# Optimization experiments

Hardware: AMD Instinct MI355X
Metric: run time of the kernel (lower is better)

The kernel has to match this reference:

```python
import jax, jax.numpy as jnp
import numpy as np

B, L, D_MODEL = 2, 1024, 512
N_LAYERS, D_STATE, D_CONV = 6, 16, 4
D_INNER = 2 * D_MODEL          # Mamba default expand=2
DT_RANK = (D_MODEL + 15) // 16  # ceil(d_model/16) = 32
EPS = 1.1920929e-07             # torch RMSNorm default eps (fp32 machine eps)


def rmsnorm(x, w):
    return x * jax.lax.rsqrt(jnp.mean(x * x, axis=-1, keepdims=True) + EPS) * w


def selective_scan(u, dt, A, Bm, Cm, Dv):
    # u, dt: (B,L,E); A: (E,N); Bm, Cm: (B,L,N); Dv: (E,)
    dA = jnp.exp(jnp.einsum('ble,en->blen', dt, A))    # discretized A (ZOH)
    dBu = jnp.einsum('ble,bln->blen', dt * u, Bm)      # discretized B * u (Euler)

    def step(h, inp):
        dA_t, dBu_t, C_t = inp
        h = dA_t * h + dBu_t                           # (B,E,N) state update
        y = jnp.einsum('ben,bn->be', h, C_t)
        return h, y

    h0 = jnp.zeros((u.shape[0], u.shape[2], A.shape[1]), u.dtype)
    _, ys = jax.lax.scan(step, h0,
                         (dA.transpose(1, 0, 2, 3), dBu.transpose(1, 0, 2, 3),
                          Cm.transpose(1, 0, 2)))
    return ys.transpose(1, 0, 2) + u * Dv


def mamba_block(x, p):
    xz = jnp.einsum('bld,ed->ble', x, p['in_proj_w'])  # (B,L,2E)
    xi, z = jnp.split(xz, 2, axis=-1)
    # causal depthwise conv1d (kernel D_CONV) + bias + SiLU
    xc = jnp.pad(xi.transpose(0, 2, 1), ((0, 0), (0, 0), (D_CONV - 1, 0)))
    xc = jax.lax.conv_general_dilated(xc, p['conv_w'][:, None, :], (1,), 'VALID',
                                      feature_group_count=D_INNER)
    xi = jax.nn.silu(xc.transpose(0, 2, 1) + p['conv_b'])
    dbc = jnp.einsum('ble,re->blr', xi, p['x_proj_w'])  # (B,L,R+2N)
    dt, Bm, Cm = jnp.split(dbc, [DT_RANK, DT_RANK + D_STATE], axis=-1)
    dt = jax.nn.softplus(jnp.einsum('blr,er->ble', dt, p['dt_w']) + p['dt_b'])
    y = selective_scan(xi, dt, -jnp.exp(p['A_log']), Bm, Cm, p['D'])
    y = y * jax.nn.silu(z)                              # gate branch
    return jnp.einsum('ble,de->bld', y, p['out_w'])


def setup_inputs() -> dict:
    key = jax.random.key(0)
    ks = jax.random.split(key, 8)
    s = 0.02
    return {
        'x': jax.random.normal(ks[0], (B, L, D_MODEL), jnp.float32),
        'position_embedding': jax.random.normal(ks[1], (B, L, D_MODEL), jnp.float32) * 0.02,
        'norm_w': jnp.ones((D_MODEL,), jnp.float32),
        'in_proj_w': jax.random.normal(ks[2], (N_LAYERS, 2 * D_INNER, D_MODEL), jnp.float32) * s,
        'conv_w': jax.random.normal(ks[3], (N_LAYERS, D_INNER, D_CONV), jnp.float32) * 0.2,
        'conv_b': jnp.zeros((N_LAYERS, D_INNER), jnp.float32),
        'x_proj_w': jax.random.normal(ks[4], (N_LAYERS, DT_RANK + 2 * D_STATE, D_INNER), jnp.float32) * s,
        'dt_w': jax.random.normal(ks[5], (N_LAYERS, D_INNER, DT_RANK), jnp.float32) * s,
        'dt_b': jnp.full((N_LAYERS, D_INNER), -4.6, jnp.float32),  # softplus(dt_b) ~ 0.01
        'A_log': jnp.broadcast_to(
            jnp.log(jnp.arange(1, D_STATE + 1, dtype=jnp.float32)),
            (N_LAYERS, D_INNER, D_STATE)) + jnp.zeros((N_LAYERS, D_INNER, D_STATE), jnp.float32),
        'D': jnp.ones((N_LAYERS, D_INNER), jnp.float32),
        'out_w': jax.random.normal(ks[6], (N_LAYERS, D_MODEL, D_INNER), jnp.float32) * s,
    }


def reference(x, position_embedding, norm_w, in_proj_w, conv_w, conv_b,
              x_proj_w, dt_w, dt_b, A_log, D, out_w):
    stacked = dict(in_proj_w=in_proj_w, conv_w=conv_w, conv_b=conv_b,
                   x_proj_w=x_proj_w, dt_w=dt_w, dt_b=dt_b,
                   A_log=A_log, D=D, out_w=out_w)

    def body(h, p):
        h = h + position_embedding          # added at the start of every layer
        h = mamba_block(rmsnorm(h, norm_w), p)  # NOTE: no residual, per source
        return h, None

    h, _ = jax.lax.scan(body, x, stacked)
    return h
```

## Files before the change

### kernel.cpp

```cpp
#include <hip/hip_runtime.h>
#include <hip/hip_bf16.h>


typedef __attribute__((ext_vector_type(8))) short bf16x8;
typedef __attribute__((ext_vector_type(4))) float f32x4;

__device__ __forceinline__ float bf2f(unsigned short u) {
    unsigned int x = ((unsigned int)u) << 16;
    return __builtin_bit_cast(float, x);
}
__device__ __forceinline__ unsigned short f2bf(float f) {
    __hip_bfloat16 h = __float2bfloat16(f);
    return __builtin_bit_cast(unsigned short, h);
}
__device__ __forceinline__ float ldin(const void* p, size_t i, int isbf) {
    return isbf ? bf2f(((const unsigned short*)p)[i]) : ((const float*)p)[i];
}
__device__ __forceinline__ float softplus_f(float x) {
    return (x > 20.f) ? x : log1pf(__expf(x));
}
__device__ __forceinline__ void split2(float x, unsigned short& h, unsigned short& l) {
    h = f2bf(x);
    l = f2bf(x - bf2f(h));
}

#define S1 (6*2048*512)
#define S2 (6*512*1024)
#define S3 (6*64*1024)
__global__ __launch_bounds__(256) void wsplit_all(
    const void* __restrict__ ipw, const void* __restrict__ ow,
    const void* __restrict__ xpw, const void* __restrict__ Dw,
    unsigned short* __restrict__ h1, unsigned short* __restrict__ l1,
    unsigned short* __restrict__ h2, unsigned short* __restrict__ l2,
    unsigned short* __restrict__ h3, unsigned short* __restrict__ l3,
    int* __restrict__ flag)
{
    int g = blockIdx.x * 256 + threadIdx.x;
    const int isbf = (*(const unsigned int*)Dw == 0x3F800000u) ? 0 : 1;
    if (g == 0) *flag = isbf;
    const void* src; unsigned short *dh, *dl; int i;
    if (g < S1)             { src = ipw; dh = h1; dl = l1; i = g; }
    else if (g < S1+S2)     { src = ow;  dh = h2; dl = l2; i = g - S1; }
    else if (g < S1+S2+S3)  { src = xpw; dh = h3; dl = l3; i = g - S1 - S2; }
    else return;
    unsigned short hh, ll;
    split2(ldin(src, i, isbf), hh, ll);
    dh[i] = hh; dl[i] = ll;
}

__global__ __launch_bounds__(256) void gemm_in(
    const unsigned short* __restrict__ Ah, const unsigned short* __restrict__ Al,
    const unsigned short* __restrict__ Wh, const unsigned short* __restrict__ Wl,
    long woff,
    float* __restrict__ xf, unsigned short* __restrict__ zg)
{
    __shared__ __align__(16) unsigned short As[2][128][40];
    __shared__ __align__(16) unsigned short Ws[2][64][40];

    const int m0 = blockIdx.x * 128, n0 = blockIdx.y * 64;
    const int t = threadIdx.x, lane = t & 63, wave = t >> 6;
    const int wm = (wave & 1) * 64, wn = (wave >> 1) * 32;
    const int sra = t >> 1, sca = (t & 1) * 16;
    const int srw = t >> 2, scw = (t & 3) * 8;

    const unsigned short* ah = Ah + (size_t)(m0 + sra) * 512 + sca;
    const unsigned short* al = Al + (size_t)(m0 + sra) * 512 + sca;
    const unsigned short* wh = Wh + woff + (size_t)(n0 + srw) * 512 + scw;
    const unsigned short* wl = Wl + woff + (size_t)(n0 + srw) * 512 + scw;

    f32x4 acc[4][2] = {};
    const int fm = lane & 15, fk = (lane >> 4) * 8;

    for (int k0 = 0; k0 < 512; k0 += 32) {
        __syncthreads();
        *(uint4*)(&As[0][sra][sca])     = *(const uint4*)(ah + k0);
        *(uint4*)(&As[0][sra][sca + 8]) = *(const uint4*)(ah + k0 + 8);
        *(uint4*)(&As[1][sra][sca])     = *(const uint4*)(al + k0);
        *(uint4*)(&As[1][sra][sca + 8]) = *(const uint4*)(al + k0 + 8);
        *(uint4*)(&Ws[0][srw][scw])     = *(const uint4*)(wh + k0);
        *(uint4*)(&Ws[1][srw][scw])     = *(const uint4*)(wl + k0);
        __syncthreads();

        bf16x8 a_h[4], a_l[4], w_h[2], w_l[2];
#pragma unroll
        for (int i = 0; i < 4; ++i) {
            a_h[i] = *(const bf16x8*)(&As[0][wm + i * 16 + fm][fk]);
            a_l[i] = *(const bf16x8*)(&As[1][wm + i * 16 + fm][fk]);
        }
#pragma unroll
        for (int i = 0; i < 2; ++i) {
            w_h[i] = *(const bf16x8*)(&Ws[0][wn + i * 16 + fm][fk]);
            w_l[i] = *(const bf16x8*)(&Ws[1][wn + i * 16 + fm][fk]);
        }
#pragma unroll
        for (int mi = 0; mi < 4; ++mi)
#pragma unroll
            for (int ni = 0; ni < 2; ++ni) {
                acc[mi][ni] = __builtin_amdgcn_mfma_f32_16x16x32_bf16(
                    a_h[mi], w_h[ni], acc[mi][ni], 0, 0, 0);
                acc[mi][ni] = __builtin_amdgcn_mfma_f32_16x16x32_bf16(
                    a_h[mi], w_l[ni], acc[mi][ni], 0, 0, 0);
                acc[mi][ni] = __builtin_amdgcn_mfma_f32_16x16x32_bf16(
                    a_l[mi], w_h[ni], acc[mi][ni], 0, 0, 0);
            }
    }

    const int col = lane & 15, rb = (lane >> 4) * 4;
    const int zhalf = (n0 >= 1024);
#pragma unroll
    for (int mi = 0; mi < 4; ++mi)
#pragma unroll
        for (int ni = 0; ni < 2; ++ni)
#pragma unroll
            for (int r = 0; r < 4; ++r) {
                int gm = m0 + wm + mi * 16 + rb + r;
                int gn = n0 + wn + ni * 16 + col;
                float v = acc[mi][ni][r];
                if (!zhalf) {
                    xf[(size_t)gm * 1024 + gn] = v;
                } else {
                    float sv = v / (1.f + __expf(-v));
                    zg[(size_t)gm * 1024 + (gn - 1024)] = f2bf(sv);
                }
            }
}

__global__ __launch_bounds__(256) void gemm_hl(
    const unsigned short* __restrict__ Ah, const unsigned short* __restrict__ Al,
    int lda,
    const unsigned short* __restrict__ Wh, const unsigned short* __restrict__ Wl,
    long woff,
    float* __restrict__ Cf, long zstride,
    int N, int K, int Kc)
{
    __shared__ __align__(16) unsigned short As[2][64][40];
    __shared__ __align__(16) unsigned short Ws[2][64][40];

    const int m0 = blockIdx.x * 64, n0 = blockIdx.y * 64;
    const int kb = blockIdx.z * Kc;
    const int t = threadIdx.x;
    const int lane = t & 63, wave = t >> 6;
    const int wm = (wave & 1) * 32, wn = (wave >> 1) * 32;
    const int srow = t >> 2, scol = (t & 3) * 8;

    const unsigned short* ah = Ah + (size_t)(m0 + srow) * lda + scol;
    const unsigned short* al = Al + (size_t)(m0 + srow) * lda + scol;
    const unsigned short* wh = Wh + woff + (size_t)(n0 + srow) * K + scol;
    const unsigned short* wl = Wl + woff + (size_t)(n0 + srow) * K + scol;

    f32x4 acc[2][2] = {};

    for (int k0 = kb; k0 < kb + Kc; k0 += 32) {
        __syncthreads();
        *(uint4*)(&As[0][srow][scol]) = *(const uint4*)(ah + k0);
        *(uint4*)(&As[1][srow][scol]) = *(const uint4*)(al + k0);
        *(uint4*)(&Ws[0][srow][scol]) = *(const uint4*)(wh + k0);
        *(uint4*)(&Ws[1][srow][scol]) = *(const uint4*)(wl + k0);
        __syncthreads();

        const int fm = lane & 15, fk = (lane >> 4) * 8;
        bf16x8 a0h = *(const bf16x8*)(&As[0][wm + fm][fk]);
        bf16x8 a1h = *(const bf16x8*)(&As[0][wm + 16 + fm][fk]);
        bf16x8 w0h = *(const bf16x8*)(&Ws[0][wn + fm][fk]);
        bf16x8 w1h = *(const bf16x8*)(&Ws[0][wn + 16 + fm][fk]);
        bf16x8 a0l = *(const bf16x8*)(&As[1][wm + fm][fk]);
        bf16x8 a1l = *(const bf16x8*)(&As[1][wm + 16 + fm][fk]);
        bf16x8 w0l = *(const bf16x8*)(&Ws[1][wn + fm][fk]);
        bf16x8 w1l = *(const bf16x8*)(&Ws[1][wn + 16 + fm][fk]);

        acc[0][0] = __builtin_amdgcn_mfma_f32_16x16x32_bf16(a0h, w0h, acc[0][0], 0, 0, 0);
        acc[0][1] = __builtin_amdgcn_mfma_f32_16x16x32_bf16(a0h, w1h, acc[0][1], 0, 0, 0);
        acc[1][0] = __builtin_amdgcn_mfma_f32_16x16x32_bf16(a1h, w0h, acc[1][0], 0, 0, 0);
        acc[1][1] = __builtin_amdgcn_mfma_f32_16x16x32_bf16(a1h, w1h, acc[1][1], 0, 0, 0);
        acc[0][0] = __builtin_amdgcn_mfma_f32_16x16x32_bf16(a0h, w0l, acc[0][0], 0, 0, 0);
        acc[0][1] = __builtin_amdgcn_mfma_f32_16x16x32_bf16(a0h, w1l, acc[0][1], 0, 0, 0);
        acc[1][0] = __builtin_amdgcn_mfma_f32_16x16x32_bf16(a1h, w0l, acc[1][0], 0, 0, 0);
        acc[1][1] = __builtin_amdgcn_mfma_f32_16x16x32_bf16(a1h, w1l, acc[1][1], 0, 0, 0);
        acc[0][0] = __builtin_amdgcn_mfma_f32_16x16x32_bf16(a0l, w0h, acc[0][0], 0, 0, 0);
        acc[0][1] = __builtin_amdgcn_mfma_f32_16x16x32_bf16(a0l, w1h, acc[0][1], 0, 0, 0);
        acc[1][0] = __builtin_amdgcn_mfma_f32_16x16x32_bf16(a1l, w0h, acc[1][0], 0, 0, 0);
        acc[1][1] = __builtin_amdgcn_mfma_f32_16x16x32_bf16(a1l, w1h, acc[1][1], 0, 0, 0);
    }

    float* Cp = Cf + (size_t)blockIdx.z * zstride;
    const int col = lane & 15, rb = (lane >> 4) * 4;
#pragma unroll
    for (int mi = 0; mi < 2; ++mi)
#pragma unroll
        for (int ni = 0; ni < 2; ++ni)
#pragma unroll
            for (int r = 0; r < 4; ++r) {
                int gm = m0 + wm + mi * 16 + rb + r;
                int gn = n0 + wn + ni * 16 + col;
                Cp[(size_t)gm * N + gn] = acc[mi][ni][r];
            }
}

__global__ __launch_bounds__(256) void dtred_k(
    const float* __restrict__ Pxp, float* __restrict__ dbc,
    const void* __restrict__ dtw, long dtwoff,
    const void* __restrict__ dtb, long dtboff,
    const int* __restrict__ flag,
    float* __restrict__ dtf)
{
    const int isbf = *flag;
    __shared__ float ldbc[16][68];
    __shared__ float ldsw[256][33];
    const int tid = threadIdx.x;
    const int e0 = blockIdx.x * 256;
    const int t0 = blockIdx.y * 16;

    {
        int tt = tid >> 4, nn = tid & 15;
        float sx = 0.f, sy = 0.f, sz = 0.f, sw = 0.f;
#pragma unroll
        for (int z = 0; z < 8; ++z) {
            const float4 v = *(const float4*)(Pxp + (size_t)z * 131072
                                              + (size_t)(t0 + tt) * 64 + nn * 4);
            sx += v.x; sy += v.y; sz += v.z; sw += v.w;
        }
        ldbc[tt][nn * 4 + 0] = sx; ldbc[tt][nn * 4 + 1] = sy;
        ldbc[tt][nn * 4 + 2] = sz; ldbc[tt][nn * 4 + 3] = sw;
        if (blockIdx.x == 0) {
            float4 o; o.x = sx; o.y = sy; o.z = sz; o.w = sw;
            *(float4*)(dbc + (size_t)(t0 + tt) * 64 + nn * 4) = o;
        }
    }
    for (int idx = tid; idx < 256 * 32; idx += 256)
        ldsw[idx >> 5][idx & 31] = ldin(dtw, dtwoff + (size_t)e0 * 32 + idx, isbf);
    __syncthreads();

    float wr[32];
#pragma unroll
    for (int r = 0; r < 32; ++r) wr[r] = ldsw[tid][r];
    float bias = ldin(dtb, dtboff + e0 + tid, isbf);

#pragma unroll
    for (int j = 0; j < 16; ++j) {
        float s = bias;
#pragma unroll
        for (int q = 0; q < 32; ++q) s += ldbc[j][q] * wr[q];
        dtf[(size_t)(t0 + j) * 1024 + e0 + tid] = softplus_f(s);
    }
}

__global__ __launch_bounds__(256) void rmsnorm_k(
    const void* __restrict__ hsrc, int hdyn, const void* __restrict__ pos,
    const void* __restrict__ nw, const int* __restrict__ flag,
    unsigned short* __restrict__ xnh, unsigned short* __restrict__ xnl)
{
    const int isbf = *flag;
    const int row = blockIdx.x;
    const int t = threadIdx.x;
    const size_t base = (size_t)row * 512;
    float h0 = hdyn ? ldin(hsrc, base + t, isbf)       : ((const float*)hsrc)[base + t];
    float h1 = hdyn ? ldin(hsrc, base + 256 + t, isbf) : ((const float*)hsrc)[base + 256 + t];
    float v0 = h0 + ldin(pos, base + t, isbf);
    float v1 = h1 + ldin(pos, base + 256 + t, isbf);
    float ss = v0 * v0 + v1 * v1;
#pragma unroll
    for (int o = 32; o; o >>= 1) ss += __shfl_xor(ss, o, 64);
    __shared__ float sw[4];
    if ((t & 63) == 0) sw[t >> 6] = ss;
    __syncthreads();
    float tot = sw[0] + sw[1] + sw[2] + sw[3];
    float sc = rsqrtf(tot * (1.0f / 512.0f) + 1.1920929e-07f);
    float o0 = v0 * sc * ldin(nw, t, isbf);
    float o1 = v1 * sc * ldin(nw, 256 + t, isbf);
    unsigned short hh, ll;
    split2(o0, hh, ll); xnh[base + t] = hh;       xnl[base + t] = ll;
    split2(o1, hh, ll); xnh[base + 256 + t] = hh; xnl[base + 256 + t] = ll;
}

__global__ __launch_bounds__(256) void conv_silu_k(
    const float* __restrict__ xf,
    const void* __restrict__ cw, long cwoff,
    const void* __restrict__ cb, long cboff,
    const int* __restrict__ flag,
    unsigned short* __restrict__ xih, unsigned short* __restrict__ xil)
{
    const int isbf = *flag;
    int g = blockIdx.x * 256 + threadIdx.x;
    int e = g & 1023;
    int l = (g >> 10) & 1023;
    int b = g >> 20;
    float acc = ldin(cb, cboff + e, isbf);
#pragma unroll
    for (int k = 0; k < 4; ++k) {
        int ls = l - 3 + k;
        if (ls >= 0)
            acc += ldin(cw, cwoff + e * 4 + k, isbf) *
                   xf[((size_t)(b * 1024 + ls)) * 1024 + e];
    }
    acc = acc / (1.f + __expf(-acc));
    unsigned short hh, ll;
    split2(acc, hh, ll);
    xih[g] = hh; xil[g] = ll;
}

#define CL 16
#define NCH 64

__global__ __launch_bounds__(256) void scan_stage1(
    const float* __restrict__ dtp,
    const unsigned short* __restrict__ xih, const unsigned short* __restrict__ xil,
    const float* __restrict__ dbc,
    const void* __restrict__ alog, long aoff, const int* __restrict__ flag,
    float* __restrict__ P, float* __restrict__ S)
{
    const int isbf = *flag;
    int bid = blockIdx.x;
    int eb = bid & 7, c = (bid >> 3) & 63, b = bid >> 9;
    int tid = threadIdx.x;
    int e = eb * 128 + (tid & 127);
    int nb = (tid >> 7) * 8;
    int t0 = b * 1024 + c * CL;

    float dv[CL], uv[CL];
#pragma unroll
    for (int i = 0; i < CL; ++i) {
        size_t ix = (size_t)(t0 + i) * 1024 + e;
        dv[i] = dtp[ix];
        uv[i] = bf2f(xih[ix]) + bf2f(xil[ix]);
    }

    float Aen[8], Pn[8], Sn[8];
#pragma unroll
    for (int n = 0; n < 8; ++n) {
        Aen[n] = -__expf(ldin(alog, aoff + e * 16 + nb + n, isbf));
        Pn[n] = 1.f; Sn[n] = 0.f;
    }
#pragma unroll
    for (int i = 0; i < CL; ++i) {
        float d = dv[i], du = d * uv[i];
        const float4* Bp = (const float4*)(dbc + (size_t)(t0 + i) * 64 + 32 + nb);
        float4 b0 = Bp[0], b1 = Bp[1];
        float Bt[8] = {b0.x, b0.y, b0.z, b0.w, b1.x, b1.y, b1.z, b1.w};
#pragma unroll
        for (int n = 0; n < 8; ++n) {
            float a = __expf(d * Aen[n]);
            Sn[n] = a * Sn[n] + du * Bt[n];
            Pn[n] *= a;
        }
    }
    size_t ob = ((size_t)(b * NCH + c) * 16 + nb) * 1024 + e;
#pragma unroll
    for (int n = 0; n < 8; ++n) {
        P[ob + (size_t)n * 1024] = Pn[n];
        S[ob + (size_t)n * 1024] = Sn[n];
    }
}

__global__ __launch_bounds__(256) void scan_stage2(
    float* __restrict__ PH, const float* __restrict__ S)
{
    int g = blockIdx.x * 256 + threadIdx.x;
    int e = g & 1023, n = (g >> 10) & 15, b = g >> 14;
    float H = 0.f;
    for (int cb = 0; cb < NCH; cb += 8) {
        float p[8], s[8];
#pragma unroll
        for (int j = 0; j < 8; ++j) {
            size_t idx = ((size_t)(b * NCH + cb + j) * 16 + n) * 1024 + e;
            p[j] = PH[idx]; s[j] = S[idx];
        }
#pragma unroll
        for (int j = 0; j < 8; ++j) {
            size_t idx = ((size_t)(b * NCH + cb + j) * 16 + n) * 1024 + e;
            PH[idx] = H;
            H = p[j] * H + s[j];
        }
    }
}

__global__ __launch_bounds__(256) void scan_stage3(
    const float* __restrict__ dtp,
    const unsigned short* __restrict__ xih, const unsigned short* __restrict__ xil,
    const float* __restrict__ dbc,
    const void* __restrict__ alog, long aoff,
    const void* __restrict__ Dv, long doff,
    const int* __restrict__ flag,
    const unsigned short* __restrict__ zg, const float* __restrict__ H0,
    unsigned short* __restrict__ yh, unsigned short* __restrict__ yl)
{
    const int isbf = *flag;
    __shared__ float ybuf[128][17];
    int bid = blockIdx.x;
    int eb = bid & 7, c = (bid >> 3) & 63, b = bid >> 9;
    int tid = threadIdx.x;
    int el = tid & 127;
    int e = eb * 128 + el;
    int half = tid >> 7;
    int nb = half * 8;
    int t0 = b * 1024 + c * CL;

    float dv[CL], uv[CL];
#pragma unroll
    for (int i = 0; i < CL; ++i) {
        size_t ix = (size_t)(t0 + i) * 1024 + e;
        dv[i] = dtp[ix];
        uv[i] = bf2f(xih[ix]) + bf2f(xil[ix]);
    }

    float Aen[8], h[8];
    size_t ob = ((size_t)(b * NCH + c) * 16 + nb) * 1024 + e;
#pragma unroll
    for (int n = 0; n < 8; ++n) {
        Aen[n] = -__expf(ldin(alog, aoff + e * 16 + nb + n, isbf));
        h[n] = H0[ob + (size_t)n * 1024];
    }

    float yv[CL];
#pragma unroll
    for (int i = 0; i < CL; ++i) {
        float d = dv[i], du = d * uv[i];
        const float4* Bp = (const float4*)(dbc + (size_t)(t0 + i) * 64 + 32 + nb);
        const float4* Cp = (const float4*)(dbc + (size_t)(t0 + i) * 64 + 48 + nb);
        float4 b0 = Bp[0], b1 = Bp[1];
        float4 c0 = Cp[0], c1 = Cp[1];
        float Bt[8] = {b0.x, b0.y, b0.z, b0.w, b1.x, b1.y, b1.z, b1.w};
        float Ct[8] = {c0.x, c0.y, c0.z, c0.w, c1.x, c1.y, c1.z, c1.w};
        float y = 0.f;
#pragma unroll
        for (int n = 0; n < 8; ++n) {
            float a = __expf(d * Aen[n]);
            h[n] = a * h[n] + du * Bt[n];
            y += h[n] * Ct[n];
        }
        yv[i] = y;
    }

    if (half == 1) {
#pragma unroll
        for (int i = 0; i < CL; ++i) ybuf[el][i] = yv[i];
    }
    __syncthreads();
    if (half == 0) {
        float De = ldin(Dv, doff + e, isbf);
#pragma unroll
        for (int i = 0; i < CL; ++i) {
            size_t ix = (size_t)(t0 + i) * 1024 + e;
            float yt = (yv[i] + ybuf[el][i] + uv[i] * De) * bf2f(zg[ix]);
            unsigned short hh, ll;
            split2(yt, hh, ll);
            yh[ix] = hh;
            yl[ix] = ll;
        }
    }
}

extern "C" void kernel_launch(void* const* d_in, const int* in_sizes, int n_in,
                              void* d_out, int out_size, void* d_ws, size_t ws_size,
                              hipStream_t stream)
{
    const void* x    = d_in[0];
    const void* pos  = d_in[1];
    const void* nw   = d_in[2];
    const void* ipw  = d_in[3];
    const void* cw   = d_in[4];
    const void* cb   = d_in[5];
    const void* xpw  = d_in[6];
    const void* dtw  = d_in[7];
    const void* dtb  = d_in[8];
    const void* alog = d_in[9];
    const void* Dw   = d_in[10];
    const void* ow   = d_in[11];

    char* w = (char*)d_ws;
    auto take = [&](size_t bytes) { char* p = w; w += (bytes + 255) & ~255ull; return p; };

    float* h    = (float*)take(2048ull * 512 * 4);
    float* xf   = (float*)take(2048ull * 1024 * 4);
    unsigned short* zg = (unsigned short*)take(2048ull * 1024 * 2);
    float* dbc  = (float*)take(2048ull * 64 * 4);
    float* dtf  = (float*)take(2048ull * 1024 * 4);
    float* P    = (float*)take(2ull * NCH * 16 * 1024 * 4);
    float* S    = (float*)take(2ull * NCH * 16 * 1024 * 4);
    float* Pxp  = (float*)take(8ull * 2048 * 64 * 4);
    unsigned short* xnh = (unsigned short*)take(2048ull * 512 * 2);
    unsigned short* xnl = (unsigned short*)take(2048ull * 512 * 2);
    unsigned short* xih = (unsigned short*)take(2048ull * 1024 * 2);
    unsigned short* xil = (unsigned short*)take(2048ull * 1024 * 2);
    unsigned short* yh  = (unsigned short*)take(2048ull * 1024 * 2);
    unsigned short* yl  = (unsigned short*)take(2048ull * 1024 * 2);
    unsigned short* wip_h = (unsigned short*)take(6ull * 2048 * 512 * 2);
    unsigned short* wip_l = (unsigned short*)take(6ull * 2048 * 512 * 2);
    unsigned short* wow_h = (unsigned short*)take(6ull * 512 * 1024 * 2);
    unsigned short* wow_l = (unsigned short*)take(6ull * 512 * 1024 * 2);
    unsigned short* wxp_h = (unsigned short*)take(6ull * 64 * 1024 * 2);
    unsigned short* wxp_l = (unsigned short*)take(6ull * 64 * 1024 * 2);
    int* flag = (int*)take(256);

    wsplit_all<<<(S1 + S2 + S3 + 255) / 256, 256, 0, stream>>>(
        ipw, ow, xpw, Dw,
        wip_h, wip_l, wow_h, wow_l, wxp_h, wxp_l, flag);

    for (int l = 0; l < 6; ++l) {
        rmsnorm_k<<<2048, 256, 0, stream>>>(
            l == 0 ? x : (const void*)h, l == 0 ? 1 : 0, pos, nw, flag, xnh, xnl);
        gemm_in<<<dim3(16, 32), 256, 0, stream>>>(
            xnh, xnl, wip_h, wip_l, (long)l * 2048 * 512, xf, zg);
        conv_silu_k<<<8192, 256, 0, stream>>>(xf, cw, (long)l * 4096, cb, (long)l * 1024,
                                              flag, xih, xil);
        gemm_hl<<<dim3(32, 1, 8), 256, 0, stream>>>(
            xih, xil, 1024, wxp_h, wxp_l, (long)l * 64 * 1024,
            Pxp, 2048l * 64, 64, 1024, 128);
        dtred_k<<<dim3(4, 128), 256, 0, stream>>>(
            Pxp, dbc, dtw, (long)l * 1024 * 32, dtb, (long)l * 1024, flag, dtf);
        scan_stage1<<<1024, 256, 0, stream>>>(
            dtf, xih, xil, dbc, alog, (long)l * 16384, flag, P, S);
        scan_stage2<<<128, 256, 0, stream>>>(P, S);
        scan_stage3<<<1024, 256, 0, stream>>>(
            dtf, xih, xil, dbc, alog, (long)l * 16384,
            Dw, (long)l * 1024, flag, zg, P, yh, yl);
        float* outp = (l < 5) ? h : (float*)d_out;
        gemm_hl<<<dim3(32, 8), 256, 0, stream>>>(
            yh, yl, 1024, wow_h, wow_l, (long)l * 512 * 1024,
            outp, 0, 512, 1024, 1024);
    }
}
```

Before: 916.9 us.

## Fuse conv+SiLU into x_proj GEMM and scans, split-K out_proj

Removes the standalone conv_silu kernel and the bf16 hi/lo xi buffers. The causal depthwise conv and SiLU are now recomputed from xf inside the x_proj GEMM (split-K raised to 16) and inside both scan stages. The out_proj GEMM for layers 0-4 uses split-K 2, and its two partial sums are added in the next layer's rmsnorm; scan_stage2 also moves to 128-thread blocks. This saves one kernel launch and the xi write/read traffic, but adds redundant conv/exp arithmetic, extra xf reads and more partial-sum traffic.

```diff
diff --git a/kernel.cpp b/kernel.cpp
--- a/kernel.cpp
+++ b/kernel.cpp
@@ -125,40 +125,78 @@
             }
 }
 
-__global__ __launch_bounds__(256) void gemm_hl(
-    const unsigned short* __restrict__ Ah, const unsigned short* __restrict__ Al,
-    int lda,
+__global__ __launch_bounds__(256) void gemm_xp(
+    const float* __restrict__ xf,
+    const void* __restrict__ cw, long cwoff,
+    const void* __restrict__ cb, long cboff,
     const unsigned short* __restrict__ Wh, const unsigned short* __restrict__ Wl,
     long woff,
-    float* __restrict__ Cf, long zstride,
-    int N, int K, int Kc)
-{
+    const int* __restrict__ flag,
+    float* __restrict__ Pxp)
+{
+    const int isbf = *flag;
     __shared__ __align__(16) unsigned short As[2][64][40];
     __shared__ __align__(16) unsigned short Ws[2][64][40];
-
-    const int m0 = blockIdx.x * 64, n0 = blockIdx.y * 64;
-    const int kb = blockIdx.z * Kc;
+    __shared__ float cwl[64][5];
+    __shared__ float cbl[64];
+
+    const int m0 = blockIdx.x * 64;
+    const int kb = blockIdx.z * 64;
     const int t = threadIdx.x;
     const int lane = t & 63, wave = t >> 6;
     const int wm = (wave & 1) * 32, wn = (wave >> 1) * 32;
     const int srow = t >> 2, scol = (t & 3) * 8;
 
-    const unsigned short* ah = Ah + (size_t)(m0 + srow) * lda + scol;
-    const unsigned short* al = Al + (size_t)(m0 + srow) * lda + scol;
-    const unsigned short* wh = Wh + woff + (size_t)(n0 + srow) * K + scol;
-    const unsigned short* wl = Wl + woff + (size_t)(n0 + srow) * K + scol;
+    if (t < 64) {
+#pragma unroll
+        for (int k = 0; k < 4; ++k)
+            cwl[t][k] = ldin(cw, cwoff + (size_t)(kb + t) * 4 + k, isbf);
+        cbl[t] = ldin(cb, cboff + kb + t, isbf);
+    }
+
+    const unsigned short* wh = Wh + woff + (size_t)srow * 1024 + scol;
+    const unsigned short* wl = Wl + woff + (size_t)srow * 1024 + scol;
 
     f32x4 acc[2][2] = {};
-
-    for (int k0 = kb; k0 < kb + Kc; k0 += 32) {
+    const int trow = m0 + srow;
+    const int bb = trow >> 10, lt = trow & 1023;
+    const int fm = lane & 15, fk = (lane >> 4) * 8;
+
+    for (int k0 = 0; k0 < 64; k0 += 32) {
+        const int e0 = kb + k0 + scol;
         __syncthreads();
-        *(uint4*)(&As[0][srow][scol]) = *(const uint4*)(ah + k0);
-        *(uint4*)(&As[1][srow][scol]) = *(const uint4*)(al + k0);
-        *(uint4*)(&Ws[0][srow][scol]) = *(const uint4*)(wh + k0);
-        *(uint4*)(&Ws[1][srow][scol]) = *(const uint4*)(wl + k0);
+        {
+            float vrow[4][8];
+#pragma unroll
+            for (int r = 0; r < 4; ++r) {
+                int l2 = lt - 3 + r;
+                if (l2 >= 0) {
+                    const float* p = xf + ((size_t)(bb * 1024 + l2)) * 1024 + e0;
+                    float4 u0 = *(const float4*)p, u1 = *(const float4*)(p + 4);
+                    vrow[r][0]=u0.x; vrow[r][1]=u0.y; vrow[r][2]=u0.z; vrow[r][3]=u0.w;
+                    vrow[r][4]=u1.x; vrow[r][5]=u1.y; vrow[r][6]=u1.z; vrow[r][7]=u1.w;
+                } else {
+#pragma unroll
+                    for (int j = 0; j < 8; ++j) vrow[r][j] = 0.f;
+                }
+            }
+#pragma unroll
+            for (int j = 0; j < 8; ++j) {
+                int el = k0 + scol + j;
+                float a = cbl[el];
+#pragma unroll
+                for (int r = 0; r < 4; ++r) a += cwl[el][r] * vrow[r][j];
+                a = a / (1.f + __expf(-a));
+                unsigned short hh, ll;
+                split2(a, hh, ll);
+                As[0][srow][scol + j] = hh;
+                As[1][srow][scol + j] = ll;
+            }
+        }
+        *(uint4*)(&Ws[0][srow][scol]) = *(const uint4*)(wh + kb + k0);
+        *(uint4*)(&Ws[1][srow][scol]) = *(const uint4*)(wl + kb + k0);
         __syncthreads();
 
-        const int fm = lane & 15, fk = (lane >> 4) * 8;
         bf16x8 a0h = *(const bf16x8*)(&As[0][wm + fm][fk]);
         bf16x8 a1h = *(const bf16x8*)(&As[0][wm + 16 + fm][fk]);
         bf16x8 w0h = *(const bf16x8*)(&Ws[0][wn + fm][fk]);
@@ -182,6 +220,77 @@
         acc[1][1] = __builtin_amdgcn_mfma_f32_16x16x32_bf16(a1l, w1h, acc[1][1], 0, 0, 0);
     }
 
+    float* Cp = Pxp + (size_t)blockIdx.z * 131072;
+    const int col = lane & 15, rb = (lane >> 4) * 4;
+#pragma unroll
+    for (int mi = 0; mi < 2; ++mi)
+#pragma unroll
+        for (int ni = 0; ni < 2; ++ni)
+#pragma unroll
+            for (int r = 0; r < 4; ++r) {
+                int gm = m0 + wm + mi * 16 + rb + r;
+                int gn = wn + ni * 16 + col;
+                Cp[(size_t)gm * 64 + gn] = acc[mi][ni][r];
+            }
+}
+
+__global__ __launch_bounds__(256) void gemm_hl(
+    const unsigned short* __restrict__ Ah, const unsigned short* __restrict__ Al,
+    int lda,
+    const unsigned short* __restrict__ Wh, const unsigned short* __restrict__ Wl,
+    long woff,
+    float* __restrict__ Cf, long zstride,
+    int N, int K, int Kc)
+{
+    __shared__ __align__(16) unsigned short As[2][64][40];
+    __shared__ __align__(16) unsigned short Ws[2][64][40];
+
+    const int m0 = blockIdx.x * 64, n0 = blockIdx.y * 64;
+    const int kb = blockIdx.z * Kc;
+    const int t = threadIdx.x;
+    const int lane = t & 63, wave = t >> 6;
+    const int wm = (wave & 1) * 32, wn = (wave >> 1) * 32;
+    const int srow = t >> 2, scol = (t & 3) * 8;
+
+    const unsigned short* ah = Ah + (size_t)(m0 + srow) * lda + scol;
+    const unsigned short* al = Al + (size_t)(m0 + srow) * lda + scol;
+    const unsigned short* wh = Wh + woff + (size_t)(n0 + srow) * K + scol;
+    const unsigned short* wl = Wl + woff + (size_t)(n0 + srow) * K + scol;
+
+    f32x4 acc[2][2] = {};
+
+    for (int k0 = kb; k0 < kb + Kc; k0 += 32) {
+        __syncthreads();
+        *(uint4*)(&As[0][srow][scol]) = *(const uint4*)(ah + k0);
+        *(uint4*)(&As[1][srow][scol]) = *(const uint4*)(al + k0);
+        *(uint4*)(&Ws[0][srow][scol]) = *(const uint4*)(wh + k0);
+        *(uint4*)(&Ws[1][srow][scol]) = *(const uint4*)(wl + k0);
+        __syncthreads();
+
+        const int fm = lane & 15, fk = (lane >> 4) * 8;
+        bf16x8 a0h = *(const bf16x8*)(&As[0][wm + fm][fk]);
+        bf16x8 a1h = *(const bf16x8*)(&As[0][wm + 16 + fm][fk]);
+        bf16x8 w0h = *(const bf16x8*)(&Ws[0][wn + fm][fk]);
+        bf16x8 w1h = *(const bf16x8*)(&Ws[0][wn + 16 + fm][fk]);
+        bf16x8 a0l = *(const bf16x8*)(&As[1][wm + fm][fk]);
+        bf16x8 a1l = *(const bf16x8*)(&As[1][wm + 16 + fm][fk]);
+        bf16x8 w0l = *(const bf16x8*)(&Ws[1][wn + fm][fk]);
+        bf16x8 w1l = *(const bf16x8*)(&Ws[1][wn + 16 + fm][fk]);
+
+        acc[0][0] = __builtin_amdgcn_mfma_f32_16x16x32_bf16(a0h, w0h, acc[0][0], 0, 0, 0);
+        acc[0][1] = __builtin_amdgcn_mfma_f32_16x16x32_bf16(a0h, w1h, acc[0][1], 0, 0, 0);
+        acc[1][0] = __builtin_amdgcn_mfma_f32_16x16x32_bf16(a1h, w0h, acc[1][0], 0, 0, 0);
+        acc[1][1] = __builtin_amdgcn_mfma_f32_16x16x32_bf16(a1h, w1h, acc[1][1], 0, 0, 0);
+        acc[0][0] = __builtin_amdgcn_mfma_f32_16x16x32_bf16(a0h, w0l, acc[0][0], 0, 0, 0);
+        acc[0][1] = __builtin_amdgcn_mfma_f32_16x16x32_bf16(a0h, w1l, acc[0][1], 0, 0, 0);
+        acc[1][0] = __builtin_amdgcn_mfma_f32_16x16x32_bf16(a1h, w0l, acc[1][0], 0, 0, 0);
+        acc[1][1] = __builtin_amdgcn_mfma_f32_16x16x32_bf16(a1h, w1l, acc[1][1], 0, 0, 0);
+        acc[0][0] = __builtin_amdgcn_mfma_f32_16x16x32_bf16(a0l, w0h, acc[0][0], 0, 0, 0);
+        acc[0][1] = __builtin_amdgcn_mfma_f32_16x16x32_bf16(a0l, w1h, acc[0][1], 0, 0, 0);
+        acc[1][0] = __builtin_amdgcn_mfma_f32_16x16x32_bf16(a1l, w0h, acc[1][0], 0, 0, 0);
+        acc[1][1] = __builtin_amdgcn_mfma_f32_16x16x32_bf16(a1l, w1h, acc[1][1], 0, 0, 0);
+    }
+
     float* Cp = Cf + (size_t)blockIdx.z * zstride;
     const int col = lane & 15, rb = (lane >> 4) * 4;
 #pragma unroll
@@ -214,7 +323,7 @@
         int tt = tid >> 4, nn = tid & 15;
         float sx = 0.f, sy = 0.f, sz = 0.f, sw = 0.f;
 #pragma unroll
-        for (int z = 0; z < 8; ++z) {
+        for (int z = 0; z < 16; ++z) {
             const float4 v = *(const float4*)(Pxp + (size_t)z * 131072
                                               + (size_t)(t0 + tt) * 64 + nn * 4);
             sx += v.x; sy += v.y; sz += v.z; sw += v.w;
@@ -245,7 +354,8 @@
 }
 
 __global__ __launch_bounds__(256) void rmsnorm_k(
-    const void* __restrict__ hsrc, int hdyn, const void* __restrict__ pos,
+    const void* __restrict__ p0, const float* __restrict__ p1, int hdyn,
+    const void* __restrict__ pos,
     const void* __restrict__ nw, const int* __restrict__ flag,
     unsigned short* __restrict__ xnh, unsigned short* __restrict__ xnl)
 {
@@ -253,8 +363,9 @@
     const int row = blockIdx.x;
     const int t = threadIdx.x;
     const size_t base = (size_t)row * 512;
-    float h0 = hdyn ? ldin(hsrc, base + t, isbf)       : ((const float*)hsrc)[base + t];
-    float h1 = hdyn ? ldin(hsrc, base + 256 + t, isbf) : ((const float*)hsrc)[base + 256 + t];
+    float h0 = hdyn ? ldin(p0, base + t, isbf)       : ((const float*)p0)[base + t];
+    float h1 = hdyn ? ldin(p0, base + 256 + t, isbf) : ((const float*)p0)[base + 256 + t];
+    if (p1) { h0 += p1[base + t]; h1 += p1[base + 256 + t]; }
     float v0 = h0 + ldin(pos, base + t, isbf);
     float v1 = h1 + ldin(pos, base + 256 + t, isbf);
     float ss = v0 * v0 + v1 * v1;
@@ -272,38 +383,13 @@
     split2(o1, hh, ll); xnh[base + 256 + t] = hh; xnl[base + 256 + t] = ll;
 }
 
-__global__ __launch_bounds__(256) void conv_silu_k(
-    const float* __restrict__ xf,
+#define CL 16
+#define NCH 64
+
+__global__ __launch_bounds__(256) void scan_stage1(
+    const float* __restrict__ dtp, const float* __restrict__ xf,
     const void* __restrict__ cw, long cwoff,
     const void* __restrict__ cb, long cboff,
-    const int* __restrict__ flag,
-    unsigned short* __restrict__ xih, unsigned short* __restrict__ xil)
-{
-    const int isbf = *flag;
-    int g = blockIdx.x * 256 + threadIdx.x;
-    int e = g & 1023;
-    int l = (g >> 10) & 1023;
-    int b = g >> 20;
-    float acc = ldin(cb, cboff + e, isbf);
-#pragma unroll
-    for (int k = 0; k < 4; ++k) {
-        int ls = l - 3 + k;
-        if (ls >= 0)
-            acc += ldin(cw, cwoff + e * 4 + k, isbf) *
-                   xf[((size_t)(b * 1024 + ls)) * 1024 + e];
-    }
-    acc = acc / (1.f + __expf(-acc));
-    unsigned short hh, ll;
-    split2(acc, hh, ll);
-    xih[g] = hh; xil[g] = ll;
-}
-
-#define CL 16
-#define NCH 64
-
-__global__ __launch_bounds__(256) void scan_stage1(
-    const float* __restrict__ dtp,
-    const unsigned short* __restrict__ xih, const unsigned short* __restrict__ xil,
     const float* __restrict__ dbc,
     const void* __restrict__ alog, long aoff, const int* __restrict__ flag,
     float* __restrict__ P, float* __restrict__ S)
@@ -314,15 +400,22 @@
     int tid = threadIdx.x;
     int e = eb * 128 + (tid & 127);
     int nb = (tid >> 7) * 8;
-    int t0 = b * 1024 + c * CL;
-
-    float dv[CL], uv[CL];
-#pragma unroll
-    for (int i = 0; i < CL; ++i) {
-        size_t ix = (size_t)(t0 + i) * 1024 + e;
-        dv[i] = dtp[ix];
-        uv[i] = bf2f(xih[ix]) + bf2f(xil[ix]);
-    }
+    int lt0 = c * CL;
+    int t0 = b * 1024 + lt0;
+
+    float dv[CL], xv[CL + 3];
+#pragma unroll
+    for (int i = 0; i < CL; ++i)
+        dv[i] = dtp[(size_t)(t0 + i) * 1024 + e];
+#pragma unroll
+    for (int i = 0; i < CL + 3; ++i) {
+        int lt = lt0 - 3 + i;
+        xv[i] = (lt >= 0) ? xf[((size_t)(b * 1024 + lt)) * 1024 + e] : 0.f;
+    }
+    float cwe[4];
+#pragma unroll
+    for (int r = 0; r < 4; ++r) cwe[r] = ldin(cw, cwoff + (size_t)e * 4 + r, isbf);
+    float cbe = ldin(cb, cboff + e, isbf);
 
     float Aen[8], Pn[8], Sn[8];
 #pragma unroll
@@ -332,7 +425,9 @@
     }
 #pragma unroll
     for (int i = 0; i < CL; ++i) {
-        float d = dv[i], du = d * uv[i];
+        float uu = cbe + cwe[0]*xv[i] + cwe[1]*xv[i+1] + cwe[2]*xv[i+2] + cwe[3]*xv[i+3];
+        uu = uu / (1.f + __expf(-uu));
+        float d = dv[i], du = d * uu;
         const float4* Bp = (const float4*)(dbc + (size_t)(t0 + i) * 64 + 32 + nb);
         float4 b0 = Bp[0], b1 = Bp[1];
         float Bt[8] = {b0.x, b0.y, b0.z, b0.w, b1.x, b1.y, b1.z, b1.w};
@@ -351,10 +446,10 @@
     }
 }
 
-__global__ __launch_bounds__(256) void scan_stage2(
+__global__ __launch_bounds__(128) void scan_stage2(
     float* __restrict__ PH, const float* __restrict__ S)
 {
-    int g = blockIdx.x * 256 + threadIdx.x;
+    int g = blockIdx.x * 128 + threadIdx.x;
     int e = g & 1023, n = (g >> 10) & 15, b = g >> 14;
     float H = 0.f;
     for (int cb = 0; cb < NCH; cb += 8) {
@@ -374,8 +469,9 @@
 }
 
 __global__ __launch_bounds__(256) void scan_stage3(
-    const float* __restrict__ dtp,
-    const unsigned short* __restrict__ xih, const unsigned short* __restrict__ xil,
+    const float* __restrict__ dtp, const float* __restrict__ xf,
+    const void* __restrict__ cw, long cwoff,
+    const void* __restrict__ cb, long cboff,
     const float* __restrict__ dbc,
     const void* __restrict__ alog, long aoff,
     const void* __restrict__ Dv, long doff,
@@ -392,15 +488,22 @@
     int e = eb * 128 + el;
     int half = tid >> 7;
     int nb = half * 8;
-    int t0 = b * 1024 + c * CL;
-
-    float dv[CL], uv[CL];
-#pragma unroll
-    for (int i = 0; i < CL; ++i) {
-        size_t ix = (size_t)(t0 + i) * 1024 + e;
-        dv[i] = dtp[ix];
-        uv[i] = bf2f(xih[ix]) + bf2f(xil[ix]);
-    }
+    int lt0 = c * CL;
+    int t0 = b * 1024 + lt0;
+
+    float dv[CL], xv[CL + 3];
+#pragma unroll
+    for (int i = 0; i < CL; ++i)
+        dv[i] = dtp[(size_t)(t0 + i) * 1024 + e];
+#pragma unroll
+    for (int i = 0; i < CL + 3; ++i) {
+        int lt = lt0 - 3 + i;
+        xv[i] = (lt >= 0) ? xf[((size_t)(b * 1024 + lt)) * 1024 + e] : 0.f;
+    }
+    float cwe[4];
+#pragma unroll
+    for (int r = 0; r < 4; ++r) cwe[r] = ldin(cw, cwoff + (size_t)e * 4 + r, isbf);
+    float cbe = ldin(cb, cboff + e, isbf);
 
     float Aen[8], h[8];
     size_t ob = ((size_t)(b * NCH + c) * 16 + nb) * 1024 + e;
@@ -413,7 +516,9 @@
     float yv[CL];
 #pragma unroll
     for (int i = 0; i < CL; ++i) {
-        float d = dv[i], du = d * uv[i];
+        float uu = cbe + cwe[0]*xv[i] + cwe[1]*xv[i+1] + cwe[2]*xv[i+2] + cwe[3]*xv[i+3];
+        uu = uu / (1.f + __expf(-uu));
+        float d = dv[i], du = d * uu;
         const float4* Bp = (const float4*)(dbc + (size_t)(t0 + i) * 64 + 32 + nb);
         const float4* Cp = (const float4*)(dbc + (size_t)(t0 + i) * 64 + 48 + nb);
         float4 b0 = Bp[0], b1 = Bp[1];
@@ -440,7 +545,9 @@
 #pragma unroll
         for (int i = 0; i < CL; ++i) {
             size_t ix = (size_t)(t0 + i) * 1024 + e;
-            float yt = (yv[i] + ybuf[el][i] + uv[i] * De) * bf2f(zg[ix]);
+            float uu = cbe + cwe[0]*xv[i] + cwe[1]*xv[i+1] + cwe[2]*xv[i+2] + cwe[3]*xv[i+3];
+            uu = uu / (1.f + __expf(-uu));
+            float yt = (yv[i] + ybuf[el][i] + uu * De) * bf2f(zg[ix]);
             unsigned short hh, ll;
             split2(yt, hh, ll);
             yh[ix] = hh;
@@ -469,18 +576,16 @@
     char* w = (char*)d_ws;
     auto take = [&](size_t bytes) { char* p = w; w += (bytes + 255) & ~255ull; return p; };
 
-    float* h    = (float*)take(2048ull * 512 * 4);
+    float* Po   = (float*)take(2ull * 2048 * 512 * 4);
     float* xf   = (float*)take(2048ull * 1024 * 4);
     unsigned short* zg = (unsigned short*)take(2048ull * 1024 * 2);
     float* dbc  = (float*)take(2048ull * 64 * 4);
     float* dtf  = (float*)take(2048ull * 1024 * 4);
     float* P    = (float*)take(2ull * NCH * 16 * 1024 * 4);
     float* S    = (float*)take(2ull * NCH * 16 * 1024 * 4);
-    float* Pxp  = (float*)take(8ull * 2048 * 64 * 4);
+    float* Pxp  = (float*)take(16ull * 2048 * 64 * 4);
     unsigned short* xnh = (unsigned short*)take(2048ull * 512 * 2);
     unsigned short* xnl = (unsigned short*)take(2048ull * 512 * 2);
-    unsigned short* xih = (unsigned short*)take(2048ull * 1024 * 2);
-    unsigned short* xil = (unsigned short*)take(2048ull * 1024 * 2);
     unsigned short* yh  = (unsigned short*)take(2048ull * 1024 * 2);
     unsigned short* yl  = (unsigned short*)take(2048ull * 1024 * 2);
     unsigned short* wip_h = (unsigned short*)take(6ull * 2048 * 512 * 2);
@@ -496,26 +601,32 @@
         wip_h, wip_l, wow_h, wow_l, wxp_h, wxp_l, flag);
 
     for (int l = 0; l < 6; ++l) {
-        rmsnorm_k<<<2048, 256, 0, stream>>>(
-            l == 0 ? x : (const void*)h, l == 0 ? 1 : 0, pos, nw, flag, xnh, xnl);
+        if (l == 0)
+            rmsnorm_k<<<2048, 256, 0, stream>>>(x, nullptr, 1, pos, nw, flag, xnh, xnl);
+        else
+            rmsnorm_k<<<2048, 256, 0, stream>>>(Po, Po + 1048576, 0, pos, nw, flag,
+                                                xnh, xnl);
         gemm_in<<<dim3(16, 32), 256, 0, stream>>>(
             xnh, xnl, wip_h, wip_l, (long)l * 2048 * 512, xf, zg);
-        conv_silu_k<<<8192, 256, 0, stream>>>(xf, cw, (long)l * 4096, cb, (long)l * 1024,
-                                              flag, xih, xil);
-        gemm_hl<<<dim3(32, 1, 8), 256, 0, stream>>>(
-            xih, xil, 1024, wxp_h, wxp_l, (long)l * 64 * 1024,
-            Pxp, 2048l * 64, 64, 1024, 128);
+        gemm_xp<<<dim3(32, 1, 16), 256, 0, stream>>>(
+            xf, cw, (long)l * 4096, cb, (long)l * 1024,
+            wxp_h, wxp_l, (long)l * 64 * 1024, flag, Pxp);
         dtred_k<<<dim3(4, 128), 256, 0, stream>>>(
             Pxp, dbc, dtw, (long)l * 1024 * 32, dtb, (long)l * 1024, flag, dtf);
         scan_stage1<<<1024, 256, 0, stream>>>(
-            dtf, xih, xil, dbc, alog, (long)l * 16384, flag, P, S);
-        scan_stage2<<<128, 256, 0, stream>>>(P, S);
+            dtf, xf, cw, (long)l * 4096, cb, (long)l * 1024,
+            dbc, alog, (long)l * 16384, flag, P, S);
+        scan_stage2<<<256, 128, 0, stream>>>(P, S);
         scan_stage3<<<1024, 256, 0, stream>>>(
-            dtf, xih, xil, dbc, alog, (long)l * 16384,
-            Dw, (long)l * 1024, flag, zg, P, yh, yl);
-        float* outp = (l < 5) ? h : (float*)d_out;
-        gemm_hl<<<dim3(32, 8), 256, 0, stream>>>(
-            yh, yl, 1024, wow_h, wow_l, (long)l * 512 * 1024,
-            outp, 0, 512, 1024, 1024);
-    }
-}
+            dtf, xf, cw, (long)l * 4096, cb, (long)l * 1024,
+            dbc, alog, (long)l * 16384, Dw, (long)l * 1024, flag, zg, P, yh, yl);
+        if (l < 5)
+            gemm_hl<<<dim3(32, 8, 2), 256, 0, stream>>>(
+                yh, yl, 1024, wow_h, wow_l, (long)l * 512 * 1024,
+                Po, 1048576, 512, 1024, 512);
+        else
+            gemm_hl<<<dim3(32, 8, 1), 256, 0, stream>>>(
+                yh, yl, 1024, wow_h, wow_l, (long)l * 512 * 1024,
+                (float*)d_out, 0, 512, 1024, 1024);
+    }
+}
```

Measured after the change: 870.6 us. -5.0%, faster.
